# Kernel optimization log

Hardware: AMD Instinct MI355X
Metric: run time of the kernel (lower is better)

The kernel has to match this reference:

```python
import jax, jax.numpy as jnp
import numpy as np

B, T, N, E = 8, 16, 2048, 32768
F_IN, C, EDGE_DIM = 32, 32, 1


def setup_inputs() -> dict:
    key = jax.random.key(0)
    ks = jax.random.split(key, 12)
    s = 1.0 / np.sqrt(C)
    x = jax.random.normal(ks[0], (B, T, N, F_IN), jnp.float32)
    edge_index = jax.random.randint(ks[1], (2, E), 0, N)
    edge_attr = jax.random.normal(ks[2], (E, EDGE_DIM), jnp.float32)
    Wl = jax.random.normal(ks[3], (F_IN, C), jnp.float32) * s
    bl = jnp.zeros((C,), jnp.float32)
    Wr = jax.random.normal(ks[4], (F_IN, C), jnp.float32) * s
    br = jnp.zeros((C,), jnp.float32)
    We = jax.random.normal(ks[5], (EDGE_DIM, C), jnp.float32) * s
    att = jax.random.normal(ks[6], (C,), jnp.float32) * s
    out_bias = jnp.zeros((C,), jnp.float32)
    w_ih = jax.random.normal(ks[7], (3 * C, C), jnp.float32) * s
    w_hh = jax.random.normal(ks[8], (3 * C, C), jnp.float32) * s
    b_ih = jnp.zeros((3 * C,), jnp.float32)
    b_hh = jnp.zeros((3 * C,), jnp.float32)
    return dict(x=x, edge_index=edge_index, edge_attr=edge_attr, Wl=Wl, bl=bl,
                Wr=Wr, br=br, We=We, att=att, out_bias=out_bias,
                w_ih=w_ih, w_hh=w_hh, b_ih=b_ih, b_hh=b_hh)


def _gatv2(x, edge_index, edge_attr, Wl, bl, Wr, br, We, att, out_bias):
    # x: [B,T,N,F]; GATv2Conv, heads=1, negative_slope=0.2, self loops w/ mean edge attr
    n = x.shape[2]
    src, dst = edge_index[0], edge_index[1]
    deg = jax.ops.segment_sum(jnp.ones((src.shape[0],), x.dtype), dst, num_segments=n)
    mean_attr = jax.ops.segment_sum(edge_attr, dst, num_segments=n) / jnp.maximum(deg, 1.0)[:, None]
    loop = jnp.arange(n)
    src_a = jnp.concatenate([src, loop])
    dst_a = jnp.concatenate([dst, loop])
    attr_a = jnp.concatenate([edge_attr, mean_attr], axis=0)
    xl = x @ Wl + bl  # [B,T,N,C]
    xr = x @ Wr + br
    e_emb = attr_a @ We  # [E2,C]
    xls = jnp.take(xl, src_a, axis=2)  # [B,T,E2,C]
    m = jax.nn.leaky_relu(xls + jnp.take(xr, dst_a, axis=2) + e_emb, 0.2)
    s = jnp.einsum('btec,c->ebt', m, att)  # [E2,B,T]
    smax = jax.ops.segment_max(s, dst_a, num_segments=n)
    es = jnp.exp(s - smax[dst_a])
    denom = jax.ops.segment_sum(es, dst_a, num_segments=n)
    alpha = es / denom[dst_a]  # segment softmax over incoming edges, [E2,B,T]
    msg = xls * alpha.transpose(1, 2, 0)[..., None]  # [B,T,E2,C]
    out = jax.ops.segment_sum(msg.transpose(2, 0, 1, 3), dst_a, num_segments=n)
    return out.transpose(1, 2, 0, 3) + out_bias  # [B,T,N,C]


def _gru(seq, w_ih, w_hh, b_ih, b_hh):
    # seq: [BN, T, C]; torch GRU gate order r,z,n
    c = seq.shape[-1]

    def step(h, xt):
        gi = xt @ w_ih.T + b_ih
        gh = h @ w_hh.T + b_hh
        ir, iz, inn = jnp.split(gi, 3, axis=-1)
        hr, hz, hn = jnp.split(gh, 3, axis=-1)
        r = jax.nn.sigmoid(ir + hr)
        z = jax.nn.sigmoid(iz + hz)
        nc = jnp.tanh(inn + r * hn)
        h = (1.0 - z) * nc + z * h
        return h, h

    h0 = jnp.zeros((seq.shape[0], c), seq.dtype)
    _, ys = jax.lax.scan(step, h0, seq.transpose(1, 0, 2))
    return ys.transpose(1, 0, 2)


def reference(x, edge_index, edge_attr, Wl, bl, Wr, br, We, att, out_bias, w_ih, w_hh, b_ih, b_hh):
    b, t, n, _ = x.shape
    h = _gatv2(x, edge_index, edge_attr, Wl, bl, Wr, br, We, att, out_bias)
    seq = h.transpose(0, 2, 1, 3).reshape(b * n, t, -1)
    y = _gru(seq, w_ih, w_hh, b_ih, b_hh)
    return y.reshape(b, n, t, -1).transpose(0, 2, 1, 3)
```

## Files before the change

### kernel.cpp

```cpp
#include <hip/hip_runtime.h>
#include <hip/hip_bf16.h>

#define N_NODES 2048
#define N_EDGES 32768
#define BT      128
#define TT      16
#define CH      32
#define E2      (N_EDGES + N_NODES)

static __device__ __forceinline__ unsigned pk2(float a, float b) {
    __hip_bfloat162 h2(__float2bfloat16(a), __float2bfloat16(b));
    return *reinterpret_cast<unsigned*>(&h2);
}

__global__ void deg_attr_kernel(const int* __restrict__ ei,
                                const float* __restrict__ ea,
                                int* __restrict__ deg, float* __restrict__ asum) {
    int e = blockIdx.x * 256 + threadIdx.x;
    if (e < N_EDGES) {
        int dst = ei[N_EDGES + e];
        atomicAdd(&deg[dst], 1);
        atomicAdd(&asum[dst], ea[e]);
    }
}

__global__ void scan_kernel(const int* __restrict__ deg, int* __restrict__ rowp) {
    int lane = threadIdx.x;
    int base = lane * 32;
    int loc[32];
    int s = 0;
    #pragma unroll
    for (int i = 0; i < 32; ++i) { loc[i] = s; s += deg[base + i] + 1; }
    int inc = s;
    #pragma unroll
    for (int d = 1; d < 64; d <<= 1) {
        int v = __shfl_up(inc, d, 64);
        if (lane >= d) inc += v;
    }
    int excl = inc - s;
    #pragma unroll
    for (int i = 0; i < 32; ++i) rowp[base + i] = excl + loc[i];
    if (lane == 63) rowp[N_NODES] = inc;
}

__global__ void scatter_kernel(const int* __restrict__ ei,
                               const float* __restrict__ ea,
                               const int* __restrict__ deg, const float* __restrict__ asum,
                               const int* __restrict__ rowp, int* __restrict__ fill,
                               int* __restrict__ col, float* __restrict__ attr_s) {
    int e = blockIdx.x * 256 + threadIdx.x;
    if (e >= E2) return;
    int src, dst; float a;
    if (e < N_EDGES) {
        src = ei[e]; dst = ei[N_EDGES + e]; a = ea[e];
    } else {
        int n = e - N_EDGES;
        src = n; dst = n;
        a = asum[n] / fmaxf((float)deg[n], 1.0f);
    }
    int pos = atomicAdd(&fill[dst], 1);
    col[rowp[dst] + pos]    = src;
    attr_s[rowp[dst] + pos] = a;
}

__global__ __launch_bounds__(256) void proj_kernel(
        const float* __restrict__ x,
        const float* __restrict__ Wl, const float* __restrict__ bl,
        const float* __restrict__ Wr, const float* __restrict__ br,
        unsigned* __restrict__ xlt, unsigned* __restrict__ xrt) {
    __shared__ float xs[128 * 32];
    __shared__ float wl[1024], wr[1024];
    int n = blockIdx.x;
    int tid = threadIdx.x;
    for (int i = tid; i < 1024; i += 256) { wl[i] = Wl[i]; wr[i] = Wr[i]; }
    #pragma unroll
    for (int i = 0; i < 16; ++i) {
        int e = i * 256 + tid;
        int bt = e >> 5, f = e & 31;
        xs[e] = x[((long)bt * N_NODES + n) * 32 + f];
    }
    __syncthreads();
    int c2  = tid & 15;
    int btl = tid >> 4;
    int c0 = 2 * c2, c1 = c0 + 1;
    float bl0 = bl[c0], bl1 = bl[c1];
    float br0 = br[c0], br1 = br[c1];
    for (int i = 0; i < 8; ++i) {
        int bt = i * 16 + btl;
        float a0 = 0.f, a1 = 0.f, r0 = 0.f, r1 = 0.f;
        #pragma unroll
        for (int f = 0; f < 32; ++f) {
            float xv = xs[bt * 32 + f];
            a0 = fmaf(xv, wl[f * 32 + c0], a0);
            a1 = fmaf(xv, wl[f * 32 + c1], a1);
            r0 = fmaf(xv, wr[f * 32 + c0], r0);
            r1 = fmaf(xv, wr[f * 32 + c1], r1);
        }
        long o = (long)n * 2048 + (bt >> 5) * 512 + (bt & 31) * 16 + c2;
        xlt[o] = pk2(a0 + bl0, a1 + bl1);
        xrt[o] = pk2(r0 + br0, r1 + br1);
    }
}

__global__ __launch_bounds__(256) void gat_kernel(
        const unsigned* __restrict__ xlt,
        const unsigned* __restrict__ xrt,
        const int* __restrict__ rowp, const int* __restrict__ col,
        const float* __restrict__ attr_s,
        const float* __restrict__ We, const float* __restrict__ att,
        const float* __restrict__ ob,
        const float* __restrict__ wih, const float* __restrict__ bih,
        __hip_bfloat16* __restrict__ gi) {
    int tid  = threadIdx.x;
    int wv   = tid >> 6;
    int lane = tid & 63;
    int epar = lane >> 5;
    int btl  = lane & 31;
    int bid  = blockIdx.x;
    int xcd  = bid & 7;
    int btq  = xcd >> 1;
    int n    = ((xcd & 1) << 10) | ((bid >> 3) << 2) | wv;
    int bt   = (btq << 5) | btl;

    long rowo = (long)n * 2048 + btq * 512 + btl * 16;

    float xrv[32];
    {
        const uint4* rp = (const uint4*)(xrt + rowo);
        uint4 A = rp[0], B = rp[1], C = rp[2], D = rp[3];
        unsigned u[16];
        u[0]=A.x; u[1]=A.y; u[2]=A.z;  u[3]=A.w;
        u[4]=B.x; u[5]=B.y; u[6]=B.z;  u[7]=B.w;
        u[8]=C.x; u[9]=C.y; u[10]=C.z; u[11]=C.w;
        u[12]=D.x; u[13]=D.y; u[14]=D.z; u[15]=D.w;
        #pragma unroll
        for (int c2 = 0; c2 < 16; ++c2) {
            xrv[2*c2]   = __uint_as_float(u[c2] << 16);
            xrv[2*c2+1] = __uint_as_float(u[c2] & 0xffff0000u);
        }
    }

    float accv[32];
    #pragma unroll
    for (int c = 0; c < 32; ++c) accv[c] = 0.f;
    float den = 0.f;

    int beg = rowp[n];
    int end = rowp[n + 1];
    const unsigned* xqbase = xlt + (long)btq * 512 + btl * 16;

    for (int j = beg + epar; j < end; j += 2) {
        int   src = col[j];
        float av  = attr_s[j];
        const uint4* gp = (const uint4*)(xqbase + (long)src * 2048);
        uint4 A = gp[0], B = gp[1], C = gp[2], D = gp[3];
        unsigned u[16];
        u[0]=A.x; u[1]=A.y; u[2]=A.z;  u[3]=A.w;
        u[4]=B.x; u[5]=B.y; u[6]=B.z;  u[7]=B.w;
        u[8]=C.x; u[9]=C.y; u[10]=C.z; u[11]=C.w;
        u[12]=D.x; u[13]=D.y; u[14]=D.z; u[15]=D.w;

        float p0 = 0.f, p1 = 0.f, p2 = 0.f, p3 = 0.f;
        #pragma unroll
        for (int c2 = 0; c2 < 16; ++c2) {
            unsigned w2 = u[c2];
            float x0 = __uint_as_float(w2 << 16);
            float x1 = __uint_as_float(w2 & 0xffff0000u);
            int c = 2 * c2;
            float m0 = x0 + fmaf(av, We[c],     xrv[c]);
            float m1 = x1 + fmaf(av, We[c + 1], xrv[c + 1]);
            if (c2 & 1) { p2 = fmaf(att[c], fmaxf(m0, 0.2f * m0), p2);
                          p3 = fmaf(att[c + 1], fmaxf(m1, 0.2f * m1), p3); }
            else        { p0 = fmaf(att[c], fmaxf(m0, 0.2f * m0), p0);
                          p1 = fmaf(att[c + 1], fmaxf(m1, 0.2f * m1), p1); }
        }
        float p = fminf((p0 + p1) + (p2 + p3), 80.f);
        float w = __expf(p);
        den += w;
        #pragma unroll
        for (int c2 = 0; c2 < 16; ++c2) {
            unsigned w2 = u[c2];
            accv[2*c2]   = fmaf(w, __uint_as_float(w2 << 16),         accv[2*c2]);
            accv[2*c2+1] = fmaf(w, __uint_as_float(w2 & 0xffff0000u), accv[2*c2+1]);
        }
    }
    den += __shfl_xor(den, 32, 64);
    #pragma unroll
    for (int c = 0; c < 32; ++c) accv[c] += __shfl_xor(accv[c], 32, 64);

    float inv = 1.f / den;
    #pragma unroll
    for (int c = 0; c < 32; ++c) accv[c] = fmaf(accv[c], inv, ob[c]);

    __hip_bfloat16* gip = gi + ((long)bt * N_NODES + n) * 96;
    int g8lo = epar * 6, g8hi = g8lo + 6;
    for (int g8 = g8lo; g8 < g8hi; ++g8) {
        float s0 = bih[g8*8+0], s1 = bih[g8*8+1], s2 = bih[g8*8+2], s3 = bih[g8*8+3];
        float s4 = bih[g8*8+4], s5 = bih[g8*8+5], s6 = bih[g8*8+6], s7 = bih[g8*8+7];
        #pragma unroll
        for (int f = 0; f < 32; ++f) {
            float hf = accv[f];
            s0 = fmaf(hf, wih[(g8*8+0)*32+f], s0);
            s1 = fmaf(hf, wih[(g8*8+1)*32+f], s1);
            s2 = fmaf(hf, wih[(g8*8+2)*32+f], s2);
            s3 = fmaf(hf, wih[(g8*8+3)*32+f], s3);
            s4 = fmaf(hf, wih[(g8*8+4)*32+f], s4);
            s5 = fmaf(hf, wih[(g8*8+5)*32+f], s5);
            s6 = fmaf(hf, wih[(g8*8+6)*32+f], s6);
            s7 = fmaf(hf, wih[(g8*8+7)*32+f], s7);
        }
        uint4 v;
        v.x = pk2(s0, s1); v.y = pk2(s2, s3); v.z = pk2(s4, s5); v.w = pk2(s6, s7);
        *(uint4*)(gip + g8 * 8) = v;
    }
}

__global__ __launch_bounds__(256) void gru_kernel(
        const float* __restrict__ whh, const float* __restrict__ bhh,
        const __hip_bfloat16* __restrict__ gi,
        float* __restrict__ out) {
    int tid  = threadIdx.x;
    int lane = tid & 63;
    int c    = lane & 31;
    int half = lane >> 5;
    int fbase = half << 4;
    int seq  = blockIdx.x * 4 + (tid >> 6);
    int b = seq >> 11;
    int n = seq & 2047;

    float w0[16], w1[16], w2[16];
    #pragma unroll
    for (int k4 = 0; k4 < 4; ++k4) {
        float4 a0 = *(const float4*)&whh[( 0 + c) * 32 + fbase + k4 * 4];
        float4 a1 = *(const float4*)&whh[(32 + c) * 32 + fbase + k4 * 4];
        float4 a2 = *(const float4*)&whh[(64 + c) * 32 + fbase + k4 * 4];
        w0[k4*4+0]=a0.x; w0[k4*4+1]=a0.y; w0[k4*4+2]=a0.z; w0[k4*4+3]=a0.w;
        w1[k4*4+0]=a1.x; w1[k4*4+1]=a1.y; w1[k4*4+2]=a1.z; w1[k4*4+3]=a1.w;
        w2[k4*4+0]=a2.x; w2[k4*4+1]=a2.y; w2[k4*4+2]=a2.z; w2[k4*4+3]=a2.w;
    }
    float bh0 = half ? 0.f : bhh[c];
    float bh1 = half ? 0.f : bhh[32 + c];
    float bh2 = half ? 0.f : bhh[64 + c];

    const long GSTR = (long)N_NODES * 96;
    long gbase = ((long)b * TT * N_NODES + n) * 96 + c;
    const long OSTR = (long)N_NODES * CH;
    long obase = ((long)b * TT * N_NODES + n) * CH + c;

    float hc = 0.f;
    float gr = __bfloat162float(gi[gbase]);
    float gz = __bfloat162float(gi[gbase + 32]);
    float gn = __bfloat162float(gi[gbase + 64]);
    #pragma unroll 1
    for (int t = 0; t < TT; ++t) {
        long gnx = gbase + (long)(t + 1) * GSTR;
        float grn = 0.f, gzn = 0.f, gnn = 0.f;
        if (t + 1 < TT) {
            grn = __bfloat162float(gi[gnx]);
            gzn = __bfloat162float(gi[gnx + 32]);
            gnn = __bfloat162float(gi[gnx + 64]);
        }
        float g0 = bh0, g1 = bh1, g2 = bh2;
        #pragma unroll
        for (int k = 0; k < 16; ++k) {
            float v = __shfl(hc, fbase + k, 64);
            g0 = fmaf(v, w0[k], g0);
            g1 = fmaf(v, w1[k], g1);
            g2 = fmaf(v, w2[k], g2);
        }
        float G0 = g0 + __shfl_xor(g0, 32, 64);
        float G1 = g1 + __shfl_xor(g1, 32, 64);
        float G2 = g2 + __shfl_xor(g2, 32, 64);
        float r  = 1.f / (1.f + __expf(-(gr + G0)));
        float z  = 1.f / (1.f + __expf(-(gz + G1)));
        float a  = fmaf(r, G2, gn);
        float e2 = __expf(2.f * a);
        float nc = 1.f - 2.f / (e2 + 1.f);
        hc = (1.f - z) * nc + z * hc;
        if (half == 0) out[obase + (long)t * OSTR] = hc;
        gr = grn; gz = gzn; gn = gnn;
    }
}

extern "C" void kernel_launch(void* const* d_in, const int* in_sizes, int n_in,
                              void* d_out, int out_size, void* d_ws, size_t ws_size,
                              hipStream_t stream) {
    const float* x    = (const float*)d_in[0];
    const int*   ei   = (const int*)d_in[1];
    const float* ea   = (const float*)d_in[2];
    const float* Wl   = (const float*)d_in[3];
    const float* bl   = (const float*)d_in[4];
    const float* Wr   = (const float*)d_in[5];
    const float* br   = (const float*)d_in[6];
    const float* We   = (const float*)d_in[7];
    const float* att  = (const float*)d_in[8];
    const float* ob   = (const float*)d_in[9];
    const float* wih  = (const float*)d_in[10];
    const float* whh  = (const float*)d_in[11];
    const float* bih  = (const float*)d_in[12];
    const float* bhh  = (const float*)d_in[13];
    float* out = (float*)d_out;

    int*   deg  = (int*)d_ws;
    float* asum = (float*)(deg + N_NODES);
    int*   fill = (int*)(asum + N_NODES);
    int*   rowp = fill + N_NODES;
    int*   col  = rowp + (N_NODES + 16);
    float* attr_s = (float*)(col + E2);
    unsigned* xlt = (unsigned*)(attr_s + E2);
    xlt = (unsigned*)(((uintptr_t)xlt + 255) & ~(uintptr_t)255);
    unsigned* xrt = xlt + (long)N_NODES * 2048;
    __hip_bfloat16* gi = (__hip_bfloat16*)(xrt + (long)N_NODES * 2048);

    hipMemsetAsync(deg, 0, 3 * N_NODES * sizeof(int), stream);

    deg_attr_kernel<<<N_EDGES / 256, 256, 0, stream>>>(ei, ea, deg, asum);
    scan_kernel<<<1, 64, 0, stream>>>(deg, rowp);
    scatter_kernel<<<(E2 + 255) / 256, 256, 0, stream>>>(ei, ea, deg, asum, rowp, fill, col, attr_s);
    proj_kernel<<<N_NODES, 256, 0, stream>>>(x, Wl, bl, Wr, br, xlt, xrt);
    gat_kernel<<<2048, 256, 0, stream>>>(xlt, xrt, rowp, col, attr_s,
                                         We, att, ob, wih, bih, gi);
    gru_kernel<<<(BT / TT * N_NODES) / 4, 256, 0, stream>>>(whh, bhh, gi, out);
}
```

Measured before the change: 283.2 us.

## Split GAT channels across half-waves and route GRU input projection through LDS

The GAT kernel now gives each block one destination node with all 128 batch-time rows. Each lane handles 16 channels instead of splitting edges by parity, and the attention logit is combined across lane halves with a shuffle per edge. Per-lane register state and gathered bytes per edge are halved, and We/att are hoisted into registers. The aggregated features are transposed through shared memory so each thread computes half of the 96 input-gate outputs for one bt. The cost is a shuffle per edge, serial edge iteration per lane, and the loss of the previous XCD-aware block mapping.

```diff
diff --git a/kernel.cpp b/kernel.cpp
--- a/kernel.cpp
+++ b/kernel.cpp
@@ -96,7 +96,7 @@
             r0 = fmaf(xv, wr[f * 32 + c0], r0);
             r1 = fmaf(xv, wr[f * 32 + c1], r1);
         }
-        long o = (long)n * 2048 + (bt >> 5) * 512 + (bt & 31) * 16 + c2;
+        long o = ((long)n * 128 + bt) * 16 + c2;
         xlt[o] = pk2(a0 + bl0, a1 + bl1);
         xrt[o] = pk2(r0 + br0, r1 + br1);
     }
@@ -111,103 +111,108 @@
         const float* __restrict__ ob,
         const float* __restrict__ wih, const float* __restrict__ bih,
         __hip_bfloat16* __restrict__ gi) {
-    int tid  = threadIdx.x;
-    int wv   = tid >> 6;
-    int lane = tid & 63;
-    int epar = lane >> 5;
-    int btl  = lane & 31;
-    int bid  = blockIdx.x;
-    int xcd  = bid & 7;
-    int btq  = xcd >> 1;
-    int n    = ((xcd & 1) << 10) | ((bid >> 3) << 2) | wv;
-    int bt   = (btq << 5) | btl;
-
-    long rowo = (long)n * 2048 + btq * 512 + btl * 16;
-
-    float xrv[32];
+    __shared__ float hsh[32 * 129];
+    int tid   = threadIdx.x;
+    int wv    = tid >> 6;
+    int lane  = tid & 63;
+    int chalf = lane >> 5;
+    int btl   = lane & 31;
+    int n     = blockIdx.x;
+    int bt    = (wv << 5) | btl;
+    int fbase = chalf << 4;
+
+    float wec[16], attc[16], xrv[16];
+    #pragma unroll
+    for (int k4 = 0; k4 < 4; ++k4) {
+        float4 w = *(const float4*)&We[fbase + k4 * 4];
+        float4 a = *(const float4*)&att[fbase + k4 * 4];
+        wec[k4*4+0]=w.x;  wec[k4*4+1]=w.y;  wec[k4*4+2]=w.z;  wec[k4*4+3]=w.w;
+        attc[k4*4+0]=a.x; attc[k4*4+1]=a.y; attc[k4*4+2]=a.z; attc[k4*4+3]=a.w;
+    }
+    long laneoff = (long)bt * 16 + chalf * 8;
     {
-        const uint4* rp = (const uint4*)(xrt + rowo);
-        uint4 A = rp[0], B = rp[1], C = rp[2], D = rp[3];
-        unsigned u[16];
-        u[0]=A.x; u[1]=A.y; u[2]=A.z;  u[3]=A.w;
-        u[4]=B.x; u[5]=B.y; u[6]=B.z;  u[7]=B.w;
-        u[8]=C.x; u[9]=C.y; u[10]=C.z; u[11]=C.w;
-        u[12]=D.x; u[13]=D.y; u[14]=D.z; u[15]=D.w;
-        #pragma unroll
-        for (int c2 = 0; c2 < 16; ++c2) {
+        const uint4* rp = (const uint4*)(xrt + (long)n * 2048 + laneoff);
+        uint4 A = rp[0], B = rp[1];
+        unsigned u[8] = {A.x, A.y, A.z, A.w, B.x, B.y, B.z, B.w};
+        #pragma unroll
+        for (int c2 = 0; c2 < 8; ++c2) {
             xrv[2*c2]   = __uint_as_float(u[c2] << 16);
             xrv[2*c2+1] = __uint_as_float(u[c2] & 0xffff0000u);
         }
     }
 
-    float accv[32];
-    #pragma unroll
-    for (int c = 0; c < 32; ++c) accv[c] = 0.f;
+    float accv[16];
+    #pragma unroll
+    for (int k = 0; k < 16; ++k) accv[k] = 0.f;
     float den = 0.f;
 
-    int beg = rowp[n];
-    int end = rowp[n + 1];
-    const unsigned* xqbase = xlt + (long)btq * 512 + btl * 16;
-
-    for (int j = beg + epar; j < end; j += 2) {
+    int beg = rowp[n], end = rowp[n + 1];
+    for (int j = beg; j < end; ++j) {
         int   src = col[j];
         float av  = attr_s[j];
-        const uint4* gp = (const uint4*)(xqbase + (long)src * 2048);
-        uint4 A = gp[0], B = gp[1], C = gp[2], D = gp[3];
-        unsigned u[16];
-        u[0]=A.x; u[1]=A.y; u[2]=A.z;  u[3]=A.w;
-        u[4]=B.x; u[5]=B.y; u[6]=B.z;  u[7]=B.w;
-        u[8]=C.x; u[9]=C.y; u[10]=C.z; u[11]=C.w;
-        u[12]=D.x; u[13]=D.y; u[14]=D.z; u[15]=D.w;
-
-        float p0 = 0.f, p1 = 0.f, p2 = 0.f, p3 = 0.f;
-        #pragma unroll
-        for (int c2 = 0; c2 < 16; ++c2) {
-            unsigned w2 = u[c2];
-            float x0 = __uint_as_float(w2 << 16);
-            float x1 = __uint_as_float(w2 & 0xffff0000u);
-            int c = 2 * c2;
-            float m0 = x0 + fmaf(av, We[c],     xrv[c]);
-            float m1 = x1 + fmaf(av, We[c + 1], xrv[c + 1]);
-            if (c2 & 1) { p2 = fmaf(att[c], fmaxf(m0, 0.2f * m0), p2);
-                          p3 = fmaf(att[c + 1], fmaxf(m1, 0.2f * m1), p3); }
-            else        { p0 = fmaf(att[c], fmaxf(m0, 0.2f * m0), p0);
-                          p1 = fmaf(att[c + 1], fmaxf(m1, 0.2f * m1), p1); }
-        }
-        float p = fminf((p0 + p1) + (p2 + p3), 80.f);
-        float w = __expf(p);
+        const uint4* gp = (const uint4*)(xlt + (long)src * 2048 + laneoff);
+        uint4 A = gp[0], B = gp[1];
+        unsigned u[8] = {A.x, A.y, A.z, A.w, B.x, B.y, B.z, B.w};
+        float p = 0.f, q = 0.f;
+        #pragma unroll
+        for (int c2 = 0; c2 < 8; ++c2) {
+            float x0 = __uint_as_float(u[c2] << 16);
+            float x1 = __uint_as_float(u[c2] & 0xffff0000u);
+            int k = 2 * c2;
+            float m0 = x0 + fmaf(av, wec[k],     xrv[k]);
+            float m1 = x1 + fmaf(av, wec[k + 1], xrv[k + 1]);
+            p = fmaf(attc[k],     fmaxf(m0, 0.2f * m0), p);
+            q = fmaf(attc[k + 1], fmaxf(m1, 0.2f * m1), q);
+        }
+        float ph = p + q;
+        float pf = ph + __shfl_xor(ph, 32, 64);
+        float w = __expf(fminf(pf, 80.f));
         den += w;
         #pragma unroll
-        for (int c2 = 0; c2 < 16; ++c2) {
-            unsigned w2 = u[c2];
-            accv[2*c2]   = fmaf(w, __uint_as_float(w2 << 16),         accv[2*c2]);
-            accv[2*c2+1] = fmaf(w, __uint_as_float(w2 & 0xffff0000u), accv[2*c2+1]);
-        }
-    }
-    den += __shfl_xor(den, 32, 64);
-    #pragma unroll
-    for (int c = 0; c < 32; ++c) accv[c] += __shfl_xor(accv[c], 32, 64);
+        for (int c2 = 0; c2 < 8; ++c2) {
+            accv[2*c2]   = fmaf(w, __uint_as_float(u[c2] << 16),         accv[2*c2]);
+            accv[2*c2+1] = fmaf(w, __uint_as_float(u[c2] & 0xffff0000u), accv[2*c2+1]);
+        }
+    }
 
     float inv = 1.f / den;
     #pragma unroll
-    for (int c = 0; c < 32; ++c) accv[c] = fmaf(accv[c], inv, ob[c]);
-
-    __hip_bfloat16* gip = gi + ((long)bt * N_NODES + n) * 96;
-    int g8lo = epar * 6, g8hi = g8lo + 6;
-    for (int g8 = g8lo; g8 < g8hi; ++g8) {
-        float s0 = bih[g8*8+0], s1 = bih[g8*8+1], s2 = bih[g8*8+2], s3 = bih[g8*8+3];
-        float s4 = bih[g8*8+4], s5 = bih[g8*8+5], s6 = bih[g8*8+6], s7 = bih[g8*8+7];
+    for (int k4 = 0; k4 < 4; ++k4) {
+        float4 o = *(const float4*)&ob[fbase + k4 * 4];
+        accv[k4*4+0] = fmaf(accv[k4*4+0], inv, o.x);
+        accv[k4*4+1] = fmaf(accv[k4*4+1], inv, o.y);
+        accv[k4*4+2] = fmaf(accv[k4*4+2], inv, o.z);
+        accv[k4*4+3] = fmaf(accv[k4*4+3], inv, o.w);
+    }
+
+    #pragma unroll
+    for (int k = 0; k < 16; ++k) hsh[(fbase + k) * 129 + bt] = accv[k];
+    __syncthreads();
+
+    int bt2   = tid & 127;
+    int ghalf = tid >> 7;
+    float hv[32];
+    #pragma unroll
+    for (int f = 0; f < 32; ++f) hv[f] = hsh[f * 129 + bt2];
+
+    __hip_bfloat16* gip = gi + ((long)bt2 * N_NODES + n) * 96 + ghalf * 48;
+    const float* wih_g = wih + ghalf * 48 * 32;
+    const float* bih_g = bih + ghalf * 48;
+    #pragma unroll
+    for (int g8 = 0; g8 < 6; ++g8) {
+        float s0 = bih_g[g8*8+0], s1 = bih_g[g8*8+1], s2 = bih_g[g8*8+2], s3 = bih_g[g8*8+3];
+        float s4 = bih_g[g8*8+4], s5 = bih_g[g8*8+5], s6 = bih_g[g8*8+6], s7 = bih_g[g8*8+7];
         #pragma unroll
         for (int f = 0; f < 32; ++f) {
-            float hf = accv[f];
-            s0 = fmaf(hf, wih[(g8*8+0)*32+f], s0);
-            s1 = fmaf(hf, wih[(g8*8+1)*32+f], s1);
-            s2 = fmaf(hf, wih[(g8*8+2)*32+f], s2);
-            s3 = fmaf(hf, wih[(g8*8+3)*32+f], s3);
-            s4 = fmaf(hf, wih[(g8*8+4)*32+f], s4);
-            s5 = fmaf(hf, wih[(g8*8+5)*32+f], s5);
-            s6 = fmaf(hf, wih[(g8*8+6)*32+f], s6);
-            s7 = fmaf(hf, wih[(g8*8+7)*32+f], s7);
+            float hf = hv[f];
+            s0 = fmaf(hf, wih_g[(g8*8+0)*32+f], s0);
+            s1 = fmaf(hf, wih_g[(g8*8+1)*32+f], s1);
+            s2 = fmaf(hf, wih_g[(g8*8+2)*32+f], s2);
+            s3 = fmaf(hf, wih_g[(g8*8+3)*32+f], s3);
+            s4 = fmaf(hf, wih_g[(g8*8+4)*32+f], s4);
+            s5 = fmaf(hf, wih_g[(g8*8+5)*32+f], s5);
+            s6 = fmaf(hf, wih_g[(g8*8+6)*32+f], s6);
+            s7 = fmaf(hf, wih_g[(g8*8+7)*32+f], s7);
         }
         uint4 v;
         v.x = pk2(s0, s1); v.y = pk2(s2, s3); v.z = pk2(s4, s5); v.w = pk2(s6, s7);
@@ -318,7 +323,7 @@
     scan_kernel<<<1, 64, 0, stream>>>(deg, rowp);
     scatter_kernel<<<(E2 + 255) / 256, 256, 0, stream>>>(ei, ea, deg, asum, rowp, fill, col, attr_s);
     proj_kernel<<<N_NODES, 256, 0, stream>>>(x, Wl, bl, Wr, br, xlt, xrt);
-    gat_kernel<<<2048, 256, 0, stream>>>(xlt, xrt, rowp, col, attr_s,
-                                         We, att, ob, wih, bih, gi);
+    gat_kernel<<<N_NODES, 256, 0, stream>>>(xlt, xrt, rowp, col, attr_s,
+                                            We, att, ob, wih, bih, gi);
     gru_kernel<<<(BT / TT * N_NODES) / 4, 256, 0, stream>>>(whh, bhh, gi, out);
 }
```

Result: no change. 286.6 us (+1.2%).

## Remap GAT kernel to one node per block with LDS edge-parity reduction

Applied to the files above, without the earlier changes.

Restructures gat_kernel so each block processes a single node, with waves split across two batch-time groups of 64 lanes and two edge parities, and the parity partial sums combined through shared memory instead of lane shuffles. The XCD-aware block swizzle is removed and addressing is simplified to a flat node-major layout. The intent is fuller 64-lane utilization per gather and simpler indexing. It adds a block barrier, rounds partial accumulators to bf16, and gives up per-XCD cache partitioning of the projected features.

```diff
diff --git a/kernel.cpp b/kernel.cpp
--- a/kernel.cpp
+++ b/kernel.cpp
@@ -96,7 +96,7 @@
             r0 = fmaf(xv, wr[f * 32 + c0], r0);
             r1 = fmaf(xv, wr[f * 32 + c1], r1);
         }
-        long o = (long)n * 2048 + (bt >> 5) * 512 + (bt & 31) * 16 + c2;
+        long o = ((long)n * 128 + bt) * 16 + c2;
         xlt[o] = pk2(a0 + bl0, a1 + bl1);
         xrt[o] = pk2(r0 + br0, r1 + br1);
     }
@@ -111,28 +111,24 @@
         const float* __restrict__ ob,
         const float* __restrict__ wih, const float* __restrict__ bih,
         __hip_bfloat16* __restrict__ gi) {
+    __shared__ unsigned accp[4][64][17];
+    __shared__ float    denp[4][64];
     int tid  = threadIdx.x;
     int wv   = tid >> 6;
     int lane = tid & 63;
-    int epar = lane >> 5;
-    int btl  = lane & 31;
-    int bid  = blockIdx.x;
-    int xcd  = bid & 7;
-    int btq  = xcd >> 1;
-    int n    = ((xcd & 1) << 10) | ((bid >> 3) << 2) | wv;
-    int bt   = (btq << 5) | btl;
-
-    long rowo = (long)n * 2048 + btq * 512 + btl * 16;
+    int btg  = wv >> 1;
+    int epar = wv & 1;
+    int n    = blockIdx.x;
+    int bt   = (btg << 6) | lane;
+
+    long laneoff = (long)bt * 16;
 
     float xrv[32];
     {
-        const uint4* rp = (const uint4*)(xrt + rowo);
+        const uint4* rp = (const uint4*)(xrt + (long)n * 2048 + laneoff);
         uint4 A = rp[0], B = rp[1], C = rp[2], D = rp[3];
-        unsigned u[16];
-        u[0]=A.x; u[1]=A.y; u[2]=A.z;  u[3]=A.w;
-        u[4]=B.x; u[5]=B.y; u[6]=B.z;  u[7]=B.w;
-        u[8]=C.x; u[9]=C.y; u[10]=C.z; u[11]=C.w;
-        u[12]=D.x; u[13]=D.y; u[14]=D.z; u[15]=D.w;
+        unsigned u[16] = {A.x,A.y,A.z,A.w, B.x,B.y,B.z,B.w,
+                          C.x,C.y,C.z,C.w, D.x,D.y,D.z,D.w};
         #pragma unroll
         for (int c2 = 0; c2 < 16; ++c2) {
             xrv[2*c2]   = __uint_as_float(u[c2] << 16);
@@ -145,20 +141,14 @@
     for (int c = 0; c < 32; ++c) accv[c] = 0.f;
     float den = 0.f;
 
-    int beg = rowp[n];
-    int end = rowp[n + 1];
-    const unsigned* xqbase = xlt + (long)btq * 512 + btl * 16;
-
+    int beg = rowp[n], end = rowp[n + 1];
     for (int j = beg + epar; j < end; j += 2) {
         int   src = col[j];
         float av  = attr_s[j];
-        const uint4* gp = (const uint4*)(xqbase + (long)src * 2048);
+        const uint4* gp = (const uint4*)(xlt + (long)src * 2048 + laneoff);
         uint4 A = gp[0], B = gp[1], C = gp[2], D = gp[3];
-        unsigned u[16];
-        u[0]=A.x; u[1]=A.y; u[2]=A.z;  u[3]=A.w;
-        u[4]=B.x; u[5]=B.y; u[6]=B.z;  u[7]=B.w;
-        u[8]=C.x; u[9]=C.y; u[10]=C.z; u[11]=C.w;
-        u[12]=D.x; u[13]=D.y; u[14]=D.z; u[15]=D.w;
+        unsigned u[16] = {A.x,A.y,A.z,A.w, B.x,B.y,B.z,B.w,
+                          C.x,C.y,C.z,C.w, D.x,D.y,D.z,D.w};
 
         float p0 = 0.f, p1 = 0.f, p2 = 0.f, p3 = 0.f;
         #pragma unroll
@@ -184,30 +174,42 @@
             accv[2*c2+1] = fmaf(w, __uint_as_float(w2 & 0xffff0000u), accv[2*c2+1]);
         }
     }
-    den += __shfl_xor(den, 32, 64);
-    #pragma unroll
-    for (int c = 0; c < 32; ++c) accv[c] += __shfl_xor(accv[c], 32, 64);
+
+    #pragma unroll
+    for (int k = 0; k < 16; ++k) accp[wv][lane][k] = pk2(accv[2*k], accv[2*k+1]);
+    denp[wv][lane] = den;
+    __syncthreads();
+    int pw = wv ^ 1;
+    den += denp[pw][lane];
+    #pragma unroll
+    for (int k = 0; k < 16; ++k) {
+        unsigned u = accp[pw][lane][k];
+        accv[2*k]   += __uint_as_float(u << 16);
+        accv[2*k+1] += __uint_as_float(u & 0xffff0000u);
+    }
 
     float inv = 1.f / den;
     #pragma unroll
     for (int c = 0; c < 32; ++c) accv[c] = fmaf(accv[c], inv, ob[c]);
 
-    __hip_bfloat16* gip = gi + ((long)bt * N_NODES + n) * 96;
-    int g8lo = epar * 6, g8hi = g8lo + 6;
-    for (int g8 = g8lo; g8 < g8hi; ++g8) {
-        float s0 = bih[g8*8+0], s1 = bih[g8*8+1], s2 = bih[g8*8+2], s3 = bih[g8*8+3];
-        float s4 = bih[g8*8+4], s5 = bih[g8*8+5], s6 = bih[g8*8+6], s7 = bih[g8*8+7];
+    __hip_bfloat16* gip = gi + ((long)bt * N_NODES + n) * 96 + epar * 48;
+    const float* wih_g = wih + epar * 48 * 32;
+    const float* bih_g = bih + epar * 48;
+    #pragma unroll
+    for (int g8 = 0; g8 < 6; ++g8) {
+        float s0 = bih_g[g8*8+0], s1 = bih_g[g8*8+1], s2 = bih_g[g8*8+2], s3 = bih_g[g8*8+3];
+        float s4 = bih_g[g8*8+4], s5 = bih_g[g8*8+5], s6 = bih_g[g8*8+6], s7 = bih_g[g8*8+7];
         #pragma unroll
         for (int f = 0; f < 32; ++f) {
             float hf = accv[f];
-            s0 = fmaf(hf, wih[(g8*8+0)*32+f], s0);
-            s1 = fmaf(hf, wih[(g8*8+1)*32+f], s1);
-            s2 = fmaf(hf, wih[(g8*8+2)*32+f], s2);
-            s3 = fmaf(hf, wih[(g8*8+3)*32+f], s3);
-            s4 = fmaf(hf, wih[(g8*8+4)*32+f], s4);
-            s5 = fmaf(hf, wih[(g8*8+5)*32+f], s5);
-            s6 = fmaf(hf, wih[(g8*8+6)*32+f], s6);
-            s7 = fmaf(hf, wih[(g8*8+7)*32+f], s7);
+            s0 = fmaf(hf, wih_g[(g8*8+0)*32+f], s0);
+            s1 = fmaf(hf, wih_g[(g8*8+1)*32+f], s1);
+            s2 = fmaf(hf, wih_g[(g8*8+2)*32+f], s2);
+            s3 = fmaf(hf, wih_g[(g8*8+3)*32+f], s3);
+            s4 = fmaf(hf, wih_g[(g8*8+4)*32+f], s4);
+            s5 = fmaf(hf, wih_g[(g8*8+5)*32+f], s5);
+            s6 = fmaf(hf, wih_g[(g8*8+6)*32+f], s6);
+            s7 = fmaf(hf, wih_g[(g8*8+7)*32+f], s7);
         }
         uint4 v;
         v.x = pk2(s0, s1); v.y = pk2(s2, s3); v.z = pk2(s4, s5); v.w = pk2(s6, s7);
@@ -318,7 +320,7 @@
     scan_kernel<<<1, 64, 0, stream>>>(deg, rowp);
     scatter_kernel<<<(E2 + 255) / 256, 256, 0, stream>>>(ei, ea, deg, asum, rowp, fill, col, attr_s);
     proj_kernel<<<N_NODES, 256, 0, stream>>>(x, Wl, bl, Wr, br, xlt, xrt);
-    gat_kernel<<<2048, 256, 0, stream>>>(xlt, xrt, rowp, col, attr_s,
-                                         We, att, ob, wih, bih, gi);
+    gat_kernel<<<N_NODES, 256, 0, stream>>>(xlt, xrt, rowp, col, attr_s,
+                                            We, att, ob, wih, bih, gi);
     gru_kernel<<<(BT / TT * N_NODES) / 4, 256, 0, stream>>>(whh, bhh, gi, out);
 }
```

After: 295.3 us. +4.3%, slower.

## Transpose xl/xr to channel-major layout and remap GAT work to full wavefront per node

Applied to the files above, without the earlier changes.

Changes the projected feature layout so each channel pair is stored contiguously across the 128 batch-time slots, letting a wavefront of 64 lanes load coalesced 4-byte words per channel instead of per-lane 64-byte uint4 chunks. Each wavefront now handles one node and 64 bt values and walks all edges itself, so the cross-half shuffle reduction goes away. The grid drops from 2048 to 1024 blocks, and the gi buffer is reordered node-major so the GRU reads time steps at stride 96. Each lane now processes twice as many edges serially, and the launch has less parallelism.

```diff
diff --git a/kernel.cpp b/kernel.cpp
--- a/kernel.cpp
+++ b/kernel.cpp
@@ -96,7 +96,7 @@
             r0 = fmaf(xv, wr[f * 32 + c0], r0);
             r1 = fmaf(xv, wr[f * 32 + c1], r1);
         }
-        long o = (long)n * 2048 + (bt >> 5) * 512 + (bt & 31) * 16 + c2;
+        long o = (long)n * 2048 + c2 * 128 + bt;
         xlt[o] = pk2(a0 + bl0, a1 + bl1);
         xrt[o] = pk2(r0 + br0, r1 + br1);
     }
@@ -111,54 +111,38 @@
         const float* __restrict__ ob,
         const float* __restrict__ wih, const float* __restrict__ bih,
         __hip_bfloat16* __restrict__ gi) {
-    int tid  = threadIdx.x;
-    int wv   = tid >> 6;
-    int lane = tid & 63;
-    int epar = lane >> 5;
-    int btl  = lane & 31;
-    int bid  = blockIdx.x;
-    int xcd  = bid & 7;
-    int btq  = xcd >> 1;
-    int n    = ((xcd & 1) << 10) | ((bid >> 3) << 2) | wv;
-    int bt   = (btq << 5) | btl;
-
-    long rowo = (long)n * 2048 + btq * 512 + btl * 16;
+    int tid = threadIdx.x;
+    int wv = tid >> 6, lane = tid & 63;
+    int task = blockIdx.x * 4 + wv;
+    int n   = task >> 1;
+    int bt  = ((task & 1) << 6) | lane;
 
     float xrv[32];
     {
-        const uint4* rp = (const uint4*)(xrt + rowo);
-        uint4 A = rp[0], B = rp[1], C = rp[2], D = rp[3];
-        unsigned u[16];
-        u[0]=A.x; u[1]=A.y; u[2]=A.z;  u[3]=A.w;
-        u[4]=B.x; u[5]=B.y; u[6]=B.z;  u[7]=B.w;
-        u[8]=C.x; u[9]=C.y; u[10]=C.z; u[11]=C.w;
-        u[12]=D.x; u[13]=D.y; u[14]=D.z; u[15]=D.w;
+        const unsigned* rp = xrt + (long)n * 2048 + bt;
         #pragma unroll
         for (int c2 = 0; c2 < 16; ++c2) {
-            xrv[2*c2]   = __uint_as_float(u[c2] << 16);
-            xrv[2*c2+1] = __uint_as_float(u[c2] & 0xffff0000u);
+            unsigned u = rp[c2 * 128];
+            xrv[2*c2]   = __uint_as_float(u << 16);
+            xrv[2*c2+1] = __uint_as_float(u & 0xffff0000u);
         }
     }
 
     float accv[32];
     #pragma unroll
     for (int c = 0; c < 32; ++c) accv[c] = 0.f;
-    float den = 0.f;
 
     int beg = rowp[n];
     int end = rowp[n + 1];
-    const unsigned* xqbase = xlt + (long)btq * 512 + btl * 16;
-
-    for (int j = beg + epar; j < end; j += 2) {
+    float den = 0.f;
+    const unsigned* xbase = xlt + bt;
+    for (int j = beg; j < end; ++j) {
         int   src = col[j];
         float av  = attr_s[j];
-        const uint4* gp = (const uint4*)(xqbase + (long)src * 2048);
-        uint4 A = gp[0], B = gp[1], C = gp[2], D = gp[3];
+        const unsigned* gp = xbase + (long)src * 2048;
         unsigned u[16];
-        u[0]=A.x; u[1]=A.y; u[2]=A.z;  u[3]=A.w;
-        u[4]=B.x; u[5]=B.y; u[6]=B.z;  u[7]=B.w;
-        u[8]=C.x; u[9]=C.y; u[10]=C.z; u[11]=C.w;
-        u[12]=D.x; u[13]=D.y; u[14]=D.z; u[15]=D.w;
+        #pragma unroll
+        for (int c2 = 0; c2 < 16; ++c2) u[c2] = gp[c2 * 128];
 
         float p0 = 0.f, p1 = 0.f, p2 = 0.f, p3 = 0.f;
         #pragma unroll
@@ -184,17 +168,13 @@
             accv[2*c2+1] = fmaf(w, __uint_as_float(w2 & 0xffff0000u), accv[2*c2+1]);
         }
     }
-    den += __shfl_xor(den, 32, 64);
-    #pragma unroll
-    for (int c = 0; c < 32; ++c) accv[c] += __shfl_xor(accv[c], 32, 64);
-
     float inv = 1.f / den;
     #pragma unroll
     for (int c = 0; c < 32; ++c) accv[c] = fmaf(accv[c], inv, ob[c]);
 
-    __hip_bfloat16* gip = gi + ((long)bt * N_NODES + n) * 96;
-    int g8lo = epar * 6, g8hi = g8lo + 6;
-    for (int g8 = g8lo; g8 < g8hi; ++g8) {
+    __hip_bfloat16* gip = gi + ((long)n * 128 + bt) * 96;
+    #pragma unroll
+    for (int g8 = 0; g8 < 12; ++g8) {
         float s0 = bih[g8*8+0], s1 = bih[g8*8+1], s2 = bih[g8*8+2], s3 = bih[g8*8+3];
         float s4 = bih[g8*8+4], s5 = bih[g8*8+5], s6 = bih[g8*8+6], s7 = bih[g8*8+7];
         #pragma unroll
@@ -242,8 +222,7 @@
     float bh1 = half ? 0.f : bhh[32 + c];
     float bh2 = half ? 0.f : bhh[64 + c];
 
-    const long GSTR = (long)N_NODES * 96;
-    long gbase = ((long)b * TT * N_NODES + n) * 96 + c;
+    long gbase = ((long)n * 128 + b * TT) * 96 + c;
     const long OSTR = (long)N_NODES * CH;
     long obase = ((long)b * TT * N_NODES + n) * CH + c;
 
@@ -253,7 +232,7 @@
     float gn = __bfloat162float(gi[gbase + 64]);
     #pragma unroll 1
     for (int t = 0; t < TT; ++t) {
-        long gnx = gbase + (long)(t + 1) * GSTR;
+        long gnx = gbase + (long)(t + 1) * 96;
         float grn = 0.f, gzn = 0.f, gnn = 0.f;
         if (t + 1 < TT) {
             grn = __bfloat162float(gi[gnx]);
@@ -318,7 +297,7 @@
     scan_kernel<<<1, 64, 0, stream>>>(deg, rowp);
     scatter_kernel<<<(E2 + 255) / 256, 256, 0, stream>>>(ei, ea, deg, asum, rowp, fill, col, attr_s);
     proj_kernel<<<N_NODES, 256, 0, stream>>>(x, Wl, bl, Wr, br, xlt, xrt);
-    gat_kernel<<<2048, 256, 0, stream>>>(xlt, xrt, rowp, col, attr_s,
-                                         We, att, ob, wih, bih, gi);
+    gat_kernel<<<(N_NODES * 2) / 4, 256, 0, stream>>>(xlt, xrt, rowp, col, attr_s,
+                                                      We, att, ob, wih, bih, gi);
     gru_kernel<<<(BT / TT * N_NODES) / 4, 256, 0, stream>>>(whh, bhh, gi, out);
 }
```

New measurement: 251.0 us. -11.4%, faster.
